# Optimization experiments

Hardware: AMD Instinct MI355X
Metric: run time of the kernel (lower is better)

## Reference

```python
import jax, jax.numpy as jnp
import numpy as np

C = 64
B, H, W = 4, 64, 64


def setup_inputs() -> dict:
    key = jax.random.key(0)
    ks = jax.random.split(key, 8)
    s = 0.05
    x = jax.random.normal(ks[0], (B, C, H, W), dtype=jnp.float32)
    Wq = jax.random.normal(ks[1], (C // 4, C), dtype=jnp.float32) * s
    bq = jax.random.normal(ks[2], (C // 4,), dtype=jnp.float32) * s
    Wk = jax.random.normal(ks[3], (C // 4, C), dtype=jnp.float32) * s
    bk = jax.random.normal(ks[4], (C // 4,), dtype=jnp.float32) * s
    Wv = jax.random.normal(ks[5], (C, C), dtype=jnp.float32) * s
    bv = jax.random.normal(ks[6], (C,), dtype=jnp.float32) * s
    gamma = jax.random.normal(ks[7], (1,), dtype=jnp.float32)
    return {"x": x, "Wq": Wq, "bq": bq, "Wk": Wk, "bk": bk, "Wv": Wv, "bv": bv, "gamma": gamma}


def reference(x, Wq, bq, Wk, bk, Wv, bv, gamma):
    b, c, h, w = x.shape
    n = h * w
    xf = x.reshape(b, c, n)  # [B, C, N]
    # 1x1 convs == channel GEMMs
    q = jnp.einsum('bcn,oc->bon', xf, Wq) + bq[None, :, None]  # [B, C/4, N]
    k = jnp.einsum('bcn,oc->bon', xf, Wk) + bk[None, :, None]  # [B, C/4, N]
    v = jnp.einsum('bcn,oc->bon', xf, Wv) + bv[None, :, None]  # [B, C, N]
    # attention[b, i, j] over key positions j (no 1/sqrt(d) scaling, per source)
    scores = jnp.einsum('bci,bcj->bij', q, k)  # [B, N, N]
    attn = jax.nn.softmax(scores, axis=-1)
    out = jnp.einsum('bcj,bij->bci', v, attn)  # [B, C, N]
    out = out.reshape(b, c, h, w)
    return gamma * out + x
```

## Files before the change

### kernel.cpp

```cpp
#include <hip/hip_runtime.h>

typedef short short8  __attribute__((ext_vector_type(8)));
typedef short short4v __attribute__((ext_vector_type(4)));
typedef float f32x4   __attribute__((ext_vector_type(4)));

#define NSPLIT 8

static __device__ __forceinline__ unsigned short f2bf(float f) {
  unsigned int u = __builtin_bit_cast(unsigned int, f);
  u += 0x7fffu + ((u >> 16) & 1u);
  return (unsigned short)(u >> 16);
}
static __device__ __forceinline__ float bf2f(unsigned short u) {
  unsigned int v = ((unsigned int)u) << 16;
  return __builtin_bit_cast(float, v);
}
static __device__ __forceinline__ unsigned int pack2bf_rtz(float lo, float hi) {
  return __builtin_amdgcn_perm(__builtin_bit_cast(unsigned int, hi),
                               __builtin_bit_cast(unsigned int, lo), 0x07060302u);
}

__global__ __launch_bounds__(256) void qkv_mfma(
    const float* __restrict__ x,
    const float* __restrict__ Wq, const float* __restrict__ bq,
    const float* __restrict__ Wk, const float* __restrict__ bk,
    const float* __restrict__ Wv, const float* __restrict__ bv,
    unsigned short* __restrict__ qb, unsigned short* __restrict__ kb,
    unsigned short* __restrict__ vb)
{
  const int rt   = blockIdx.x;
  const int nt   = blockIdx.y;
  const int b    = blockIdx.z;
  const int lane = threadIdx.x & 63;
  const int wave = threadIdx.x >> 6;
  const int l15  = lane & 15;
  const int quad = lane >> 4;
  const int n    = nt * 64 + wave * 16 + l15;

  const float* wbase; const float* bias; int row0;
  if (rt == 0)      { wbase = Wq; bias = bq; row0 = 0; }
  else if (rt == 1) { wbase = Wk; bias = bk; row0 = 0; }
  else              { wbase = Wv; bias = bv; row0 = (rt - 2) * 16; }

  short8 bfrag[2];
#pragma unroll
  for (int ks = 0; ks < 2; ++ks)
#pragma unroll
    for (int jj = 0; jj < 8; ++jj) {
      const int c = ks * 32 + quad * 8 + jj;
      bfrag[ks][jj] = (short)f2bf(x[((size_t)(b * 64 + c)) * 4096 + n]);
    }

  short8 afrag[2];
#pragma unroll
  for (int ks = 0; ks < 2; ++ks) {
    f32x4 w0 = *(const f32x4*)(wbase + (row0 + l15) * 64 + ks * 32 + quad * 8);
    f32x4 w1 = *(const f32x4*)(wbase + (row0 + l15) * 64 + ks * 32 + quad * 8 + 4);
#pragma unroll
    for (int jj = 0; jj < 4; ++jj) {
      afrag[ks][jj]     = (short)f2bf(w0[jj]);
      afrag[ks][jj + 4] = (short)f2bf(w1[jj]);
    }
  }

  f32x4 acc;
#pragma unroll
  for (int r = 0; r < 4; ++r)
    acc[r] = bias[row0 + quad * 4 + r];
  acc = __builtin_amdgcn_mfma_f32_16x16x32_bf16(afrag[0], bfrag[0], acc, 0, 0, 0);
  acc = __builtin_amdgcn_mfma_f32_16x16x32_bf16(afrag[1], bfrag[1], acc, 0, 0, 0);

  if (rt <= 1) {
    if (rt == 0) {
#pragma unroll
      for (int r = 0; r < 4; ++r) acc[r] *= 1.44269504088896340736f;
    }
    short4v sv;
#pragma unroll
    for (int r = 0; r < 4; ++r) sv[r] = (short)f2bf(acc[r]);
    unsigned short* dst = (rt == 0 ? qb : kb);
    *(short4v*)(dst + (((size_t)b * 4096 + n) * 16) + quad * 4) = sv;
  } else {
#pragma unroll
    for (int r = 0; r < 4; ++r) {
      const int c = row0 + quad * 4 + r;
      vb[((size_t)(b * 64 + c)) * 4096 + n] = f2bf(acc[r]);
    }
  }
}

__global__ __launch_bounds__(256) void flash_attn(
    const unsigned short* __restrict__ qb, const unsigned short* __restrict__ kb,
    const unsigned short* __restrict__ vb,
    unsigned short* __restrict__ Opart, float* __restrict__ lpart)
{
  __shared__ unsigned short p_lds[4][64 * 64];

  const int s    = blockIdx.x;
  const int qw4  = blockIdx.y;
  const int b    = blockIdx.z;
  const int t    = threadIdx.x;
  const int wave = t >> 6;
  const int lane = t & 63;
  const int l15  = lane & 15;
  const int quad = lane >> 4;
  const int sw   = l15 & 7;
  const int qw   = qw4 * 4 + wave;

  short8 qfrag[4];
#pragma unroll
  for (int qt = 0; qt < 4; ++qt) {
    qfrag[qt] = (short8)0;
    if (quad < 2) {
      const int iq = qw * 64 + qt * 16 + l15;
      qfrag[qt] = *(const short8*)(qb + (((size_t)b * 4096 + iq) * 16 + quad * 8));
    }
  }

  const unsigned short* vbb = vb + (size_t)b * 64 * 4096;
  const unsigned short* kbb = kb + (size_t)b * 4096 * 16;
  f32x4 acc[4][4];
#pragma unroll
  for (int qt = 0; qt < 4; ++qt)
#pragma unroll
    for (int ct = 0; ct < 4; ++ct) acc[qt][ct] = (f32x4)0.f;
  float lp[4] = {0.f, 0.f, 0.f, 0.f};
  unsigned short* pw = &p_lds[wave][0];

  const int jbeg = s * (4096 / NSPLIT);
  const int jend = jbeg + 4096 / NSPLIT;

  short8 kf[4];
#pragma unroll
  for (int sub = 0; sub < 4; ++sub) {
    kf[sub] = (short8)0;
    if (quad < 2)
      kf[sub] = *(const short8*)(kbb + (size_t)(jbeg + sub * 16 + l15) * 16 + quad * 8);
  }

#pragma unroll 1
  for (int j0 = jbeg; j0 < jend; j0 += 64) {
    short8 vf[2][4];
#pragma unroll
    for (int kc = 0; kc < 2; ++kc) {
      const int vcol = j0 + kc * 32 + quad * 8;
#pragma unroll
      for (int ct = 0; ct < 4; ++ct)
        vf[kc][ct] = *(const short8*)(vbb + (size_t)(ct * 16 + l15) * 4096 + vcol);
    }

#pragma unroll
    for (int qt = 0; qt < 4; ++qt) {
#pragma unroll
      for (int sub = 0; sub < 4; ++sub) {
        f32x4 sc = __builtin_amdgcn_mfma_f32_16x16x32_bf16(kf[sub], qfrag[qt], (f32x4)0.f, 0, 0, 0);
        float p0 = exp2f(sc[0]);
        float p1 = exp2f(sc[1]);
        float p2 = exp2f(sc[2]);
        float p3 = exp2f(sc[3]);
        lp[qt] += (p0 + p1) + (p2 + p3);
        const int ch = (sub * 2 + (quad >> 1)) ^ sw;
        unsigned int* dst = (unsigned int*)(pw + (qt * 16 + l15) * 64 + ch * 8 + (quad & 1) * 4);
        dst[0] = pack2bf_rtz(p0, p1);
        dst[1] = pack2bf_rtz(p2, p3);
      }
    }

    short8 kfn[4];
    const int jn = j0 + 64;
    const bool more = (jn < jend);
#pragma unroll
    for (int sub = 0; sub < 4; ++sub) {
      kfn[sub] = (short8)0;
      if (more && quad < 2)
        kfn[sub] = *(const short8*)(kbb + (size_t)(jn + sub * 16 + l15) * 16 + quad * 8);
    }

#pragma unroll
    for (int kc = 0; kc < 2; ++kc) {
#pragma unroll
      for (int qt = 0; qt < 4; ++qt) {
        short8 pf = *(const short8*)(pw + (qt * 16 + l15) * 64 + ((kc * 4 + quad) ^ sw) * 8);
#pragma unroll
        for (int ct = 0; ct < 4; ++ct)
          acc[qt][ct] = __builtin_amdgcn_mfma_f32_16x16x32_bf16(vf[kc][ct], pf, acc[qt][ct], 0, 0, 0);
      }
    }

#pragma unroll
    for (int sub = 0; sub < 4; ++sub) kf[sub] = kfn[sub];
  }

#pragma unroll
  for (int qt = 0; qt < 4; ++qt) {
    lp[qt] += __shfl_xor(lp[qt], 16);
    lp[qt] += __shfl_xor(lp[qt], 32);
  }

  const int pslot = (b * 64 + qw) * NSPLIT + s;
  unsigned short* Op = Opart + (size_t)pslot * 4096;
#pragma unroll
  for (int qt = 0; qt < 4; ++qt)
#pragma unroll
    for (int ct = 0; ct < 4; ++ct) {
      short4v sv;
#pragma unroll
      for (int r = 0; r < 4; ++r) sv[r] = (short)f2bf(acc[qt][ct][r]);
      *(short4v*)(Op + (qt * 16 + l15) * 64 + ct * 16 + quad * 4) = sv;
    }
  if (lane < 16) {
#pragma unroll
    for (int qt = 0; qt < 4; ++qt)
      lpart[(size_t)pslot * 64 + qt * 16 + lane] = lp[qt];
  }
}

__global__ __launch_bounds__(1024) void finalize(
    const unsigned short* __restrict__ Opart, const float* __restrict__ lpart,
    const float* __restrict__ x, const float* __restrict__ gptr,
    float* __restrict__ out)
{
  __shared__ float osum[64 * 65];
  __shared__ float linv[64];

  const int qw = blockIdx.x;
  const int b  = blockIdx.y;
  const int t  = threadIdx.x;
  const int base = (b * 64 + qw) * NSPLIT;

  if (t < 64) {
    float sum = 0.f;
#pragma unroll
    for (int s = 0; s < NSPLIT; ++s) sum += lpart[(size_t)(base + s) * 64 + t];
    linv[t] = 1.f / sum;
  }

  f32x4 o = (f32x4)0.f;
  const unsigned short* Op = Opart + (size_t)base * 4096;
#pragma unroll
  for (int s = 0; s < NSPLIT; ++s) {
    short4v v = *(const short4v*)(Op + (size_t)s * 4096 + 4 * t);
#pragma unroll
    for (int r = 0; r < 4; ++r)
      o[r] += bf2f((unsigned short)v[r]);
  }

  const int q  = t >> 4;
  const int c0 = (t & 15) * 4;
#pragma unroll
  for (int r = 0; r < 4; ++r)
    osum[(c0 + r) * 65 + q] = o[r];
  __syncthreads();

  const float g  = gptr[0];
  const int   qq = t & 63;
  const float li = linv[qq];
#pragma unroll
  for (int i = 0; i < 4; ++i) {
    const int c = (t >> 6) + 16 * i;
    const size_t off = ((size_t)(b * 64 + c)) * 4096 + qw * 64 + qq;
    out[off] = g * (osum[c * 65 + qq] * li) + x[off];
  }
}

extern "C" void kernel_launch(void* const* d_in, const int* in_sizes, int n_in,
                              void* d_out, int out_size, void* d_ws, size_t ws_size,
                              hipStream_t stream)
{
  const float* x  = (const float*)d_in[0];
  const float* Wq = (const float*)d_in[1];
  const float* bq = (const float*)d_in[2];
  const float* Wk = (const float*)d_in[3];
  const float* bk = (const float*)d_in[4];
  const float* Wv = (const float*)d_in[5];
  const float* bv = (const float*)d_in[6];
  const float* g  = (const float*)d_in[7];

  unsigned short* ws = (unsigned short*)d_ws;
  unsigned short* qb = ws;
  unsigned short* kb = ws + 262144;
  unsigned short* vb = ws + 524288;
  unsigned short* Opart = (unsigned short*)((char*)d_ws + (size_t)4 * 1024 * 1024);
  float* lpart = (float*)((char*)d_ws + (size_t)24 * 1024 * 1024);
  float* ob = (float*)d_out;

  hipLaunchKernelGGL(qkv_mfma, dim3(6, 64, 4), dim3(256), 0, stream,
                     x, Wq, bq, Wk, bk, Wv, bv, qb, kb, vb);
  hipLaunchKernelGGL(flash_attn, dim3(NSPLIT, 16, 4), dim3(256), 0, stream,
                     qb, kb, vb, Opart, lpart);
  hipLaunchKernelGGL(finalize, dim3(64, 4), dim3(1024), 0, stream,
                     Opart, lpart, x, g, ob);
}
```

Baseline: 112.3 us.

## Fuse split-K attention and finalize into one block-level reduction kernel

Each block now handles one 64-query tile with 8 waves, each wave covering a 512-key slice, instead of separate blocks per split. The partial outputs and row sums are reduced in LDS with a swizzled layout, and the normalization plus residual add run in the same kernel. This removes the finalize launch and the global round-trip of bf16 partials and row sums. In exchange the grid shrinks to 256 blocks of 512 threads, and LDS use grows to 64KB per block, which may limit occupancy.

```diff
diff --git a/kernel.cpp b/kernel.cpp
--- a/kernel.cpp
+++ b/kernel.cpp
@@ -3,8 +3,6 @@
 typedef short short8  __attribute__((ext_vector_type(8)));
 typedef short short4v __attribute__((ext_vector_type(4)));
 typedef float f32x4   __attribute__((ext_vector_type(4)));
-
-#define NSPLIT 8
 
 static __device__ __forceinline__ unsigned short f2bf(float f) {
   unsigned int u = __builtin_bit_cast(unsigned int, f);
@@ -89,30 +87,29 @@
   }
 }
 
-__global__ __launch_bounds__(256) void flash_attn(
+__global__ __launch_bounds__(512) void flash_fused(
     const unsigned short* __restrict__ qb, const unsigned short* __restrict__ kb,
     const unsigned short* __restrict__ vb,
-    unsigned short* __restrict__ Opart, float* __restrict__ lpart)
+    const float* __restrict__ x, const float* __restrict__ gptr,
+    float* __restrict__ out)
 {
-  __shared__ unsigned short p_lds[4][64 * 64];
-
-  const int s    = blockIdx.x;
-  const int qw4  = blockIdx.y;
-  const int b    = blockIdx.z;
+  __shared__ unsigned short p_lds[8 * 4096];
+
+  const int qg   = blockIdx.x;
+  const int b    = blockIdx.y;
   const int t    = threadIdx.x;
   const int wave = t >> 6;
   const int lane = t & 63;
   const int l15  = lane & 15;
   const int quad = lane >> 4;
   const int sw   = l15 & 7;
-  const int qw   = qw4 * 4 + wave;
 
   short8 qfrag[4];
 #pragma unroll
   for (int qt = 0; qt < 4; ++qt) {
     qfrag[qt] = (short8)0;
     if (quad < 2) {
-      const int iq = qw * 64 + qt * 16 + l15;
+      const int iq = qg * 64 + qt * 16 + l15;
       qfrag[qt] = *(const short8*)(qb + (((size_t)b * 4096 + iq) * 16 + quad * 8));
     }
   }
@@ -125,10 +122,10 @@
 #pragma unroll
     for (int ct = 0; ct < 4; ++ct) acc[qt][ct] = (f32x4)0.f;
   float lp[4] = {0.f, 0.f, 0.f, 0.f};
-  unsigned short* pw = &p_lds[wave][0];
-
-  const int jbeg = s * (4096 / NSPLIT);
-  const int jend = jbeg + 4096 / NSPLIT;
+  unsigned short* pw = p_lds + wave * 4096;
+
+  const int jbeg = wave * 512;
+  const int jend = jbeg + 512;
 
   short8 kf[4];
 #pragma unroll
@@ -197,8 +194,6 @@
     lp[qt] += __shfl_xor(lp[qt], 32);
   }
 
-  const int pslot = (b * 64 + qw) * NSPLIT + s;
-  unsigned short* Op = Opart + (size_t)pslot * 4096;
 #pragma unroll
   for (int qt = 0; qt < 4; ++qt)
 #pragma unroll
@@ -206,60 +201,42 @@
       short4v sv;
 #pragma unroll
       for (int r = 0; r < 4; ++r) sv[r] = (short)f2bf(acc[qt][ct][r]);
-      *(short4v*)(Op + (qt * 16 + l15) * 64 + ct * 16 + quad * 4) = sv;
-    }
+      const int q = qt * 16 + l15;
+      const unsigned off = (unsigned)(q * 128 + (ct * 16 + quad * 4) * 2)
+                         ^ (unsigned)((q & 7) << 4);
+      *(short4v*)((char*)pw + off) = sv;
+    }
+  __syncthreads();
+
+  float o[8] = {0.f, 0.f, 0.f, 0.f, 0.f, 0.f, 0.f, 0.f};
+  const unsigned roff = (unsigned)(lane * 128 + wave * 16)
+                      ^ (unsigned)((lane & 7) << 4);
+#pragma unroll
+  for (int w = 0; w < 8; ++w) {
+    short8 v = *(const short8*)((const char*)(p_lds + w * 4096) + roff);
+#pragma unroll
+    for (int r = 0; r < 8; ++r) o[r] += bf2f((unsigned short)v[r]);
+  }
+  __syncthreads();
+
+  float* lf = (float*)p_lds;
   if (lane < 16) {
 #pragma unroll
     for (int qt = 0; qt < 4; ++qt)
-      lpart[(size_t)pslot * 64 + qt * 16 + lane] = lp[qt];
-  }
-}
-
-__global__ __launch_bounds__(1024) void finalize(
-    const unsigned short* __restrict__ Opart, const float* __restrict__ lpart,
-    const float* __restrict__ x, const float* __restrict__ gptr,
-    float* __restrict__ out)
-{
-  __shared__ float osum[64 * 65];
-  __shared__ float linv[64];
-
-  const int qw = blockIdx.x;
-  const int b  = blockIdx.y;
-  const int t  = threadIdx.x;
-  const int base = (b * 64 + qw) * NSPLIT;
-
-  if (t < 64) {
-    float sum = 0.f;
-#pragma unroll
-    for (int s = 0; s < NSPLIT; ++s) sum += lpart[(size_t)(base + s) * 64 + t];
-    linv[t] = 1.f / sum;
-  }
-
-  f32x4 o = (f32x4)0.f;
-  const unsigned short* Op = Opart + (size_t)base * 4096;
-#pragma unroll
-  for (int s = 0; s < NSPLIT; ++s) {
-    short4v v = *(const short4v*)(Op + (size_t)s * 4096 + 4 * t);
-#pragma unroll
-    for (int r = 0; r < 4; ++r)
-      o[r] += bf2f((unsigned short)v[r]);
-  }
-
-  const int q  = t >> 4;
-  const int c0 = (t & 15) * 4;
-#pragma unroll
-  for (int r = 0; r < 4; ++r)
-    osum[(c0 + r) * 65 + q] = o[r];
+      lf[wave * 64 + qt * 16 + lane] = lp[qt];
+  }
   __syncthreads();
-
+  float lsum = 0.f;
+#pragma unroll
+  for (int w = 0; w < 8; ++w) lsum += lf[w * 64 + lane];
+  const float li = 1.f / lsum;
   const float g  = gptr[0];
-  const int   qq = t & 63;
-  const float li = linv[qq];
-#pragma unroll
-  for (int i = 0; i < 4; ++i) {
-    const int c = (t >> 6) + 16 * i;
-    const size_t off = ((size_t)(b * 64 + c)) * 4096 + qw * 64 + qq;
-    out[off] = g * (osum[c * 65 + qq] * li) + x[off];
+
+#pragma unroll
+  for (int r = 0; r < 8; ++r) {
+    const int c = wave * 8 + r;
+    const size_t off = ((size_t)(b * 64 + c)) * 4096 + (size_t)qg * 64 + lane;
+    out[off] = g * (o[r] * li) + x[off];
   }
 }
 
@@ -280,14 +257,10 @@
   unsigned short* qb = ws;
   unsigned short* kb = ws + 262144;
   unsigned short* vb = ws + 524288;
-  unsigned short* Opart = (unsigned short*)((char*)d_ws + (size_t)4 * 1024 * 1024);
-  float* lpart = (float*)((char*)d_ws + (size_t)24 * 1024 * 1024);
   float* ob = (float*)d_out;
 
   hipLaunchKernelGGL(qkv_mfma, dim3(6, 64, 4), dim3(256), 0, stream,
                      x, Wq, bq, Wk, bk, Wv, bv, qb, kb, vb);
-  hipLaunchKernelGGL(flash_attn, dim3(NSPLIT, 16, 4), dim3(256), 0, stream,
-                     qb, kb, vb, Opart, lpart);
-  hipLaunchKernelGGL(finalize, dim3(64, 4), dim3(1024), 0, stream,
-                     Opart, lpart, x, g, ob);
-}
+  hipLaunchKernelGGL(flash_fused, dim3(64, 4), dim3(512), 0, stream,
+                     qb, kb, vb, x, g, ob);
+}
```

New measurement: 103.5 us. 1.08x faster.
